# Optimization experiments

Hardware: AMD Instinct MI355X
Metric: run time of the kernel (lower is better)

The kernel has to match this reference:

```python
import jax, jax.numpy as jnp
import numpy as np
from jax import lax

NUM_C_TYPES = 6
TTYPE_UNKNOWN = 5
E = 6            # num_experts_C
D = 1024         # embed_dim
H = D // 4       # gate hidden
TOP_K = 1
TEMP = 0.1
FLOOR = min(0.05, 0.15 / 4)   # routing_floor property (num_experts_B = 4)
CAP_LOW, CAP_HIGH, T_MAX = 0.5, 0.6, 1000


def _build_base_assignment():
    base = np.zeros((NUM_C_TYPES, E), dtype=np.float32)
    for t_type in range(NUM_C_TYPES - 1):
        base[t_type, t_type % E] = 1.0
    base[TTYPE_UNKNOWN] = 1.0 / E
    num_known = NUM_C_TYPES - 1
    if E > num_known:
        for extra_idx in range(num_known, E):
            base[extra_idx % num_known, extra_idx] = 0.3
        for t_type in range(NUM_C_TYPES - 1):
            s = base[t_type].sum()
            if s > 0:
                base[t_type] /= s
    return jnp.asarray(base)


def setup_inputs() -> dict:
    key = jax.random.key(0)
    k1, k2, k3, k4, k5 = jax.random.split(key, 5)
    B, N = 8, 4096
    tokens = jax.random.normal(k1, (B, N, D), dtype=jnp.float32)
    token_types = jax.random.randint(k2, (B, N), 0, NUM_C_TYPES, dtype=jnp.int64)
    t = jax.random.randint(k3, (B,), 0, T_MAX, dtype=jnp.int64)
    # second_gate params; xavier_uniform with gain=0.01
    lim1 = 0.01 * np.sqrt(6.0 / (D + H))
    lim2 = 0.01 * np.sqrt(6.0 / (H + E))
    W1 = jax.random.uniform(k4, (D, H), minval=-lim1, maxval=lim1, dtype=jnp.float32)
    b1 = jnp.zeros((H,), dtype=jnp.float32)
    W2 = jax.random.uniform(k5, (H, E), minval=-lim2, maxval=lim2, dtype=jnp.float32)
    b2 = jnp.zeros((E,), dtype=jnp.float32)
    return {"tokens": tokens, "token_types": token_types, "t": t,
            "W1": W1, "b1": b1, "W2": W2, "b2": b2,
            "base_assignment": _build_base_assignment()}


def _hard_cap(probs, t):
    # TokenLevelHardCap.apply (note faithful cap formula: low + (high + low) * t_norm)
    t_norm = t.astype(probs.dtype) / T_MAX
    cap = (CAP_LOW + (CAP_HIGH + CAP_LOW) * t_norm)[:, None, None]  # (B,1,1)
    excess = jax.nn.relu(probs - cap)
    capped = probs - excess
    headroom = jax.nn.relu(cap - capped)
    headroom_sum = jnp.clip(headroom.sum(-1, keepdims=True), 1e-8, None)
    capped = capped + excess.sum(-1, keepdims=True) * (headroom / headroom_sum)
    return capped


def reference(tokens, token_types, t, W1, b1, W2, b2, base_assignment):
    B, N, _ = tokens.shape
    # primary: deterministic type -> expert assignment (gather)
    base_probs = base_assignment[token_types]                 # (B,N,E)
    # secondary: 2-layer MLP gate, temperature-scaled logits
    h = jax.nn.gelu(jnp.einsum('bnd,dh->bnh', tokens, W1) + b1, approximate=False)
    secondary_logits = (jnp.einsum('bnh,he->bne', h, W2) + b2) / TEMP
    is_unknown = (token_types == TTYPE_UNKNOWN)[..., None].astype(tokens.dtype)
    # faithful to source: unknown tokens blend in raw logits (not softmax probs)
    probs = (1.0 - is_unknown) * base_probs + is_unknown * secondary_logits
    # routing floor interpolation toward uniform
    alpha = min(FLOOR * E, 1.0)
    probs = (1.0 - alpha) * probs + alpha * (1.0 / E)
    # top-k scatter mask
    vals, idx = lax.top_k(probs, TOP_K)                       # (B,N,k)
    dispatch = (jax.nn.one_hot(idx, E, dtype=probs.dtype) * vals[..., None]).sum(-2)
    # no_grad hard cap with redistribution
    dispatch = lax.stop_gradient(_hard_cap(dispatch, t))
    combine = dispatch / (dispatch.sum(-1, keepdims=True) + 1e-8)
    return dispatch, combine
```

## Files before the change

kernel.cpp:

```cpp
#include <hip/hip_runtime.h>
#include <math.h>

#define NUM_E 6
#define DIM 1024
#define HID 256
#define NTOK 32768
#define NPB 4096
#define TTYPE_UNKNOWN 5
#define ONE_MINUS_ALPHA 0.775f
#define FLOOR_TERM 0.0375f
#define GRP 8
#define KSPLIT 8
#define KSPAN 128
#define CPT 4

__device__ __forceinline__ void finalize_and_write(const float probs[NUM_E], float cap,
                                                   float* __restrict__ disp_out,
                                                   float* __restrict__ comb_out) {
    float v = probs[0];
    int bi = 0;
#pragma unroll
    for (int e = 1; e < NUM_E; ++e) {
        if (probs[e] > v) { v = probs[e]; bi = e; }
    }
    float excess = fmaxf(v - cap, 0.0f);
    float capped = v - excess;
    float hr_idx = fmaxf(cap - capped, 0.0f);
    float hsum = fmaxf(hr_idx + 5.0f * cap, 1e-8f);
    float disp[NUM_E];
    float other = excess * cap / hsum;
#pragma unroll
    for (int e = 0; e < NUM_E; ++e) disp[e] = other;
    disp[bi] = capped + excess * hr_idx / hsum;
    float s = 0.0f;
#pragma unroll
    for (int e = 0; e < NUM_E; ++e) s += disp[e];
    float inv = 1.0f / (s + 1e-8f);
#pragma unroll
    for (int e = 0; e < NUM_E; ++e) {
        disp_out[e] = disp[e];
        comb_out[e] = disp[e] * inv;
    }
}

__launch_bounds__(256)
__global__ void classify_kernel(const int* __restrict__ ttypes,
                                const int* __restrict__ tarr,
                                const float* __restrict__ base,
                                float* __restrict__ out,
                                int* __restrict__ cnt,
                                int* __restrict__ list) {
    int i = blockIdx.x * blockDim.x + threadIdx.x;
    if (i >= NTOK) return;
    int ty = ttypes[i];
    if (ty == TTYPE_UNKNOWN) {
        int pos = atomicAdd(cnt, 1);
        list[pos] = i;
        return;
    }
    int b = i / NPB;
    float tnorm = (float)tarr[b] / 1000.0f;
    float cap = 0.5f + 1.1f * tnorm;
    float probs[NUM_E];
#pragma unroll
    for (int e = 0; e < NUM_E; ++e)
        probs[e] = ONE_MINUS_ALPHA * base[ty * NUM_E + e] + FLOOR_TERM;
    finalize_and_write(probs, cap,
                       out + (size_t)i * NUM_E,
                       out + (size_t)NTOK * NUM_E + (size_t)i * NUM_E);
}

__launch_bounds__(512)
__global__ void mlp_kernel(const float* __restrict__ tokens,
                           const int* __restrict__ tarr,
                           const float* __restrict__ W1,
                           const float* __restrict__ b1,
                           const float* __restrict__ W2,
                           const float* __restrict__ b2,
                           float* __restrict__ out,
                           const int* __restrict__ cnt,
                           const int* __restrict__ list) {
    __shared__ float smem[GRP * DIM];
    __shared__ float w2s[HID * NUM_E];
    __shared__ float ls[GRP][NUM_E];

    int count = cnt[0];
    int start = blockIdx.x * GRP;
    if (start >= count) return;
    int tid = threadIdx.x;

    float (*xs)[DIM] = (float (*)[DIM])smem;

    {
        int slot = tid & 255;
        int rr = tid >> 8;
#pragma unroll
        for (int p = 0; p < 4; ++p) {
            int r = rr * 4 + p;
            int idx = start + r;
            if (idx > count - 1) idx = count - 1;
            int tok = list[idx];
            const float4* src = reinterpret_cast<const float4*>(tokens + (size_t)tok * DIM);
            reinterpret_cast<float4*>(xs[r])[slot] = src[slot];
        }
    }
    for (int kk = tid; kk < HID * NUM_E; kk += 512) w2s[kk] = W2[kk];
    __syncthreads();

    int cg = tid & 63;
    int ks = tid >> 6;
    int kbase = ks * KSPAN;
    int colbase = cg * CPT;

    float acc[GRP][CPT];
#pragma unroll
    for (int r = 0; r < GRP; ++r)
#pragma unroll
        for (int c = 0; c < CPT; ++c) acc[r][c] = 0.0f;

    const float* w1p = W1 + (size_t)kbase * HID + colbase;
    const float* xbase = &xs[0][kbase];

#pragma unroll 2
    for (int k = 0; k < KSPAN; k += 4) {
        float4 w[4];
        const float* wp = w1p + (size_t)k * HID;
#pragma unroll
        for (int kk = 0; kk < 4; ++kk)
            w[kk] = *reinterpret_cast<const float4*>(wp + kk * HID);
#pragma unroll
        for (int r = 0; r < GRP; ++r) {
            float4 xq = *reinterpret_cast<const float4*>(xbase + r * DIM + k);
            acc[r][0] = fmaf(xq.x, w[0].x, acc[r][0]);
            acc[r][1] = fmaf(xq.x, w[0].y, acc[r][1]);
            acc[r][2] = fmaf(xq.x, w[0].z, acc[r][2]);
            acc[r][3] = fmaf(xq.x, w[0].w, acc[r][3]);
            acc[r][0] = fmaf(xq.y, w[1].x, acc[r][0]);
            acc[r][1] = fmaf(xq.y, w[1].y, acc[r][1]);
            acc[r][2] = fmaf(xq.y, w[1].z, acc[r][2]);
            acc[r][3] = fmaf(xq.y, w[1].w, acc[r][3]);
            acc[r][0] = fmaf(xq.z, w[2].x, acc[r][0]);
            acc[r][1] = fmaf(xq.z, w[2].y, acc[r][1]);
            acc[r][2] = fmaf(xq.z, w[2].z, acc[r][2]);
            acc[r][3] = fmaf(xq.z, w[2].w, acc[r][3]);
            acc[r][0] = fmaf(xq.w, w[3].x, acc[r][0]);
            acc[r][1] = fmaf(xq.w, w[3].y, acc[r][1]);
            acc[r][2] = fmaf(xq.w, w[3].z, acc[r][2]);
            acc[r][3] = fmaf(xq.w, w[3].w, acc[r][3]);
        }
    }
    __syncthreads();

    float (*hp)[HID] = (float (*)[HID])smem;
    float (*hs)[HID + 1] = (float (*)[HID + 1])(smem + 2048);

    const float kc = 0.70710678118654752f;
#pragma unroll 1
    for (int r = 0; r < GRP; ++r) {
#pragma unroll
        for (int c = 0; c < CPT; ++c) hp[ks][colbase + c] = acc[r][c];
        __syncthreads();
        if (tid < HID) {
            float s = hp[0][tid];
#pragma unroll
            for (int q = 1; q < KSPLIT; ++q) s += hp[q][tid];
            float pre = s + b1[tid];
            hs[r][tid] = 0.5f * pre * (1.0f + erff(pre * kc));
        }
        __syncthreads();
    }

    if (tid < GRP * NUM_E) {
        int r = tid / NUM_E, e = tid % NUM_E;
        float s = 0.0f;
        for (int j = 0; j < HID; ++j) s = fmaf(hs[r][j], w2s[j * NUM_E + e], s);
        ls[r][e] = (s + b2[e]) / 0.1f;
    }
    __syncthreads();

    if (tid < GRP && start + tid < count) {
        int tokidx = list[start + tid];
        int b = tokidx / NPB;
        float tnorm = (float)tarr[b] / 1000.0f;
        float cap = 0.5f + 1.1f * tnorm;
        float probs[NUM_E];
#pragma unroll
        for (int e = 0; e < NUM_E; ++e)
            probs[e] = ONE_MINUS_ALPHA * ls[tid][e] + FLOOR_TERM;
        finalize_and_write(probs, cap,
                           out + (size_t)tokidx * NUM_E,
                           out + (size_t)NTOK * NUM_E + (size_t)tokidx * NUM_E);
    }
}

extern "C" void kernel_launch(void* const* d_in, const int* in_sizes, int n_in,
                              void* d_out, int out_size, void* d_ws, size_t ws_size,
                              hipStream_t stream) {
    const float* tokens = (const float*)d_in[0];
    const int*   ttypes = (const int*)d_in[1];
    const int*   tarr   = (const int*)d_in[2];
    const float* W1     = (const float*)d_in[3];
    const float* b1     = (const float*)d_in[4];
    const float* W2     = (const float*)d_in[5];
    const float* b2     = (const float*)d_in[6];
    const float* base   = (const float*)d_in[7];
    float* out = (float*)d_out;

    int* cnt  = (int*)d_ws;
    int* list = (int*)d_ws + 64;

    hipMemsetAsync(cnt, 0, sizeof(int), stream);
    classify_kernel<<<NTOK / 256, 256, 0, stream>>>(ttypes, tarr, base, out, cnt, list);
    mlp_kernel<<<NTOK / GRP, 512, 0, stream>>>(tokens, tarr, W1, b1, W2, b2,
                                               out, cnt, list);
}
```

Before: 67.63 us.

## Use split-bf16 MFMA for gate MLP with fp32 recheck of near-tie tokens

Replaces the scalar FP32 first-layer GEMM for unknown tokens with MFMA bf16x3 emulation. Weights and activations are split into high and low bf16 parts, and W1 is pre-packed into an MFMA-friendly layout by a prep kernel each call. Tokens whose top-two routing probabilities are closer than a small epsilon are queued and recomputed in exact FP32 by a recheck kernel, so the argmax matches the reference. This adds two kernel launches, a weight repack and a workspace-size dependent fallback path in exchange for matrix-core throughput.

```diff
diff --git a/kernel.cpp b/kernel.cpp
--- a/kernel.cpp
+++ b/kernel.cpp
@@ -9,10 +9,19 @@
 #define TTYPE_UNKNOWN 5
 #define ONE_MINUS_ALPHA 0.775f
 #define FLOOR_TERM 0.0375f
-#define GRP 8
-#define KSPLIT 8
-#define KSPAN 128
-#define CPT 4
+#define GRPM 16
+#define EPS_GAP 2e-5f
+
+#define WS_CNT   0
+#define WS_CNT2  64
+#define WS_LIST  256
+#define WS_LIST2 (256 + 131072)
+#define WS_WFH   (512 * 1024)
+#define WS_WFL   (1024 * 1024)
+#define WS_NEED  ((size_t)(1536 * 1024))
+
+typedef __attribute__((ext_vector_type(8))) short short8;
+typedef __attribute__((ext_vector_type(4))) float f32x4;
 
 __device__ __forceinline__ void finalize_and_write(const float probs[NUM_E], float cap,
                                                    float* __restrict__ disp_out,
@@ -70,27 +79,229 @@
                        out + (size_t)NTOK * NUM_E + (size_t)i * NUM_E);
 }
 
+__launch_bounds__(256)
+__global__ void prep_w1(const float* __restrict__ W1,
+                        unsigned short* __restrict__ wfh,
+                        unsigned short* __restrict__ wfl) {
+    int idx = blockIdx.x * 256 + threadIdx.x;
+    int tg = idx >> 8;
+    int col = idx & 255;
+    int kbase = (tg >> 2) * 32 + (tg & 3) * 8;
+    unsigned int hw[4], lw[4];
+#pragma unroll
+    for (int p = 0; p < 4; ++p) {
+        unsigned int h2 = 0, l2 = 0;
+#pragma unroll
+        for (int q = 0; q < 2; ++q) {
+            int j = p * 2 + q;
+            float w = W1[(size_t)(kbase + j) * HID + col];
+            unsigned int u = __float_as_uint(w);
+            float hif = __uint_as_float(u & 0xFFFF0000u);
+            float resid = w - hif;
+            unsigned int hv = u >> 16;
+            unsigned int lv = __float_as_uint(resid) >> 16;
+            h2 |= hv << (16 * q);
+            l2 |= lv << (16 * q);
+        }
+        hw[p] = h2; lw[p] = l2;
+    }
+    size_t off = ((size_t)tg * 256 + col) * 8;
+    *reinterpret_cast<uint4*>(wfh + off) = make_uint4(hw[0], hw[1], hw[2], hw[3]);
+    *reinterpret_cast<uint4*>(wfl + off) = make_uint4(lw[0], lw[1], lw[2], lw[3]);
+}
+
+__launch_bounds__(256)
+__global__ void mfma_mlp(const float* __restrict__ tokens,
+                         const int* __restrict__ tarr,
+                         const unsigned short* __restrict__ wfh,
+                         const unsigned short* __restrict__ wfl,
+                         const float* __restrict__ b1,
+                         const float* __restrict__ W2,
+                         const float* __restrict__ b2,
+                         float* __restrict__ out,
+                         const int* __restrict__ cnt,
+                         const int* __restrict__ list,
+                         int* __restrict__ cnt2,
+                         int* __restrict__ list2) {
+    __shared__ unsigned short xh[GRPM][DIM];
+    __shared__ unsigned short xl[GRPM][DIM];
+    __shared__ float w2s[HID * NUM_E];
+    __shared__ float ls[GRPM][NUM_E];
+
+    int count = cnt[0];
+    int start = blockIdx.x * GRPM;
+    if (count == 0 || start >= count) return;
+    int tid = threadIdx.x;
+
+#pragma unroll 1
+    for (int r = 0; r < GRPM; ++r) {
+        int idx = start + r;
+        if (idx > count - 1) idx = count - 1;
+        int tok = list[idx];
+        float4 v = reinterpret_cast<const float4*>(tokens + (size_t)tok * DIM)[tid];
+        unsigned short h4[4], l4[4];
+        float xv[4] = {v.x, v.y, v.z, v.w};
+#pragma unroll
+        for (int q = 0; q < 4; ++q) {
+            unsigned int u = __float_as_uint(xv[q]);
+            float hif = __uint_as_float(u & 0xFFFF0000u);
+            float resid = xv[q] - hif;
+            h4[q] = (unsigned short)(u >> 16);
+            l4[q] = (unsigned short)(__float_as_uint(resid) >> 16);
+        }
+        *reinterpret_cast<ushort4*>(&xh[r][tid * 4]) = make_ushort4(h4[0], h4[1], h4[2], h4[3]);
+        *reinterpret_cast<ushort4*>(&xl[r][tid * 4]) = make_ushort4(l4[0], l4[1], l4[2], l4[3]);
+    }
+    for (int kk = tid; kk < HID * NUM_E; kk += 256) w2s[kk] = W2[kk];
+    __syncthreads();
+
+    int lane = tid & 63;
+    int wv = tid >> 6;
+    int arow = lane & 15;
+    int grp = lane >> 4;
+
+    f32x4 acc[4];
+#pragma unroll
+    for (int c = 0; c < 4; ++c) acc[c] = (f32x4){0.f, 0.f, 0.f, 0.f};
+
+    int colg[4];
+#pragma unroll
+    for (int c = 0; c < 4; ++c) colg[c] = wv * 64 + c * 16 + (lane & 15);
+
+#pragma unroll 1
+    for (int t = 0; t < DIM / 32; ++t) {
+        short8 ah = *reinterpret_cast<const short8*>(&xh[arow][t * 32 + grp * 8]);
+        short8 al = *reinterpret_cast<const short8*>(&xl[arow][t * 32 + grp * 8]);
+#pragma unroll
+        for (int c = 0; c < 4; ++c) {
+            size_t boff = ((size_t)(t * 4 + grp) * 256 + colg[c]) * 8;
+            short8 bh = *reinterpret_cast<const short8*>(wfh + boff);
+            short8 bl = *reinterpret_cast<const short8*>(wfl + boff);
+            acc[c] = __builtin_amdgcn_mfma_f32_16x16x32_bf16(ah, bh, acc[c], 0, 0, 0);
+            acc[c] = __builtin_amdgcn_mfma_f32_16x16x32_bf16(ah, bl, acc[c], 0, 0, 0);
+            acc[c] = __builtin_amdgcn_mfma_f32_16x16x32_bf16(al, bh, acc[c], 0, 0, 0);
+        }
+    }
+    __syncthreads();
+
+    float (*hs)[HID] = (float (*)[HID])xh;
+    const float kc = 0.70710678118654752f;
+#pragma unroll
+    for (int c = 0; c < 4; ++c) {
+        float bb = b1[colg[c]];
+#pragma unroll
+        for (int i = 0; i < 4; ++i) {
+            int row = grp * 4 + i;
+            float pre = acc[c][i] + bb;
+            hs[row][colg[c]] = 0.5f * pre * (1.0f + erff(pre * kc));
+        }
+    }
+    __syncthreads();
+
+    if (tid < GRPM * NUM_E) {
+        int r = tid / NUM_E, e = tid % NUM_E;
+        float s = 0.0f;
+        for (int j = 0; j < HID; ++j) s = fmaf(hs[r][j], w2s[j * NUM_E + e], s);
+        ls[r][e] = (s + b2[e]) / 0.1f;
+    }
+    __syncthreads();
+
+    if (tid < GRPM && start + tid < count) {
+        int tokidx = list[start + tid];
+        int b = tokidx / NPB;
+        float tnorm = (float)tarr[b] / 1000.0f;
+        float cap = 0.5f + 1.1f * tnorm;
+        float probs[NUM_E];
+#pragma unroll
+        for (int e = 0; e < NUM_E; ++e)
+            probs[e] = ONE_MINUS_ALPHA * ls[tid][e] + FLOOR_TERM;
+        float v1 = -1e30f, v2 = -1e30f;
+#pragma unroll
+        for (int e = 0; e < NUM_E; ++e) {
+            if (probs[e] > v1) { v2 = v1; v1 = probs[e]; }
+            else if (probs[e] > v2) { v2 = probs[e]; }
+        }
+        if (v1 - v2 < EPS_GAP) {
+            int p = atomicAdd(cnt2, 1);
+            list2[p] = tokidx;
+        }
+        finalize_and_write(probs, cap,
+                           out + (size_t)tokidx * NUM_E,
+                           out + (size_t)NTOK * NUM_E + (size_t)tokidx * NUM_E);
+    }
+}
+
+__launch_bounds__(256)
+__global__ void recheck_kernel(const float* __restrict__ tokens,
+                               const int* __restrict__ tarr,
+                               const float* __restrict__ W1,
+                               const float* __restrict__ b1,
+                               const float* __restrict__ W2,
+                               const float* __restrict__ b2,
+                               float* __restrict__ out,
+                               const int* __restrict__ cnt2,
+                               const int* __restrict__ list2) {
+    __shared__ float xs2[DIM];
+    __shared__ float hs2[HID];
+    __shared__ float ls2[NUM_E];
+    __shared__ float w2s2[HID * NUM_E];
+    int tid = threadIdx.x;
+    int n2 = cnt2[0];
+    if (n2 == 0) return;
+    for (int kk = tid; kk < HID * NUM_E; kk += 256) w2s2[kk] = W2[kk];
+    const float kc = 0.70710678118654752f;
+    for (int i = blockIdx.x; i < n2; i += gridDim.x) {
+        int tok = list2[i];
+        __syncthreads();
+        reinterpret_cast<float4*>(xs2)[tid] =
+            reinterpret_cast<const float4*>(tokens + (size_t)tok * DIM)[tid];
+        __syncthreads();
+        float a = 0.0f;
+        const float* wp = W1 + tid;
+#pragma unroll 8
+        for (int k = 0; k < DIM; ++k) a = fmaf(xs2[k], wp[(size_t)k * HID], a);
+        float pre = a + b1[tid];
+        hs2[tid] = 0.5f * pre * (1.0f + erff(pre * kc));
+        __syncthreads();
+        if (tid < NUM_E) {
+            float s = 0.0f;
+            for (int j = 0; j < HID; ++j) s = fmaf(hs2[j], w2s2[j * NUM_E + tid], s);
+            ls2[tid] = (s + b2[tid]) / 0.1f;
+        }
+        __syncthreads();
+        if (tid == 0) {
+            int b = tok / NPB;
+            float tnorm = (float)tarr[b] / 1000.0f;
+            float cap = 0.5f + 1.1f * tnorm;
+            float probs[NUM_E];
+#pragma unroll
+            for (int e = 0; e < NUM_E; ++e)
+                probs[e] = ONE_MINUS_ALPHA * ls2[e] + FLOOR_TERM;
+            finalize_and_write(probs, cap,
+                               out + (size_t)tok * NUM_E,
+                               out + (size_t)NTOK * NUM_E + (size_t)tok * NUM_E);
+        }
+    }
+}
+
 __launch_bounds__(512)
-__global__ void mlp_kernel(const float* __restrict__ tokens,
-                           const int* __restrict__ tarr,
-                           const float* __restrict__ W1,
-                           const float* __restrict__ b1,
-                           const float* __restrict__ W2,
-                           const float* __restrict__ b2,
-                           float* __restrict__ out,
-                           const int* __restrict__ cnt,
-                           const int* __restrict__ list) {
-    __shared__ float smem[GRP * DIM];
+__global__ void mlp_fallback(const float* __restrict__ tokens,
+                             const int* __restrict__ tarr,
+                             const float* __restrict__ W1,
+                             const float* __restrict__ b1,
+                             const float* __restrict__ W2,
+                             const float* __restrict__ b2,
+                             float* __restrict__ out,
+                             const int* __restrict__ cnt,
+                             const int* __restrict__ list) {
+    __shared__ float smem[8 * DIM];
     __shared__ float w2s[HID * NUM_E];
-    __shared__ float ls[GRP][NUM_E];
-
+    __shared__ float ls[8][NUM_E];
     int count = cnt[0];
-    int start = blockIdx.x * GRP;
-    if (start >= count) return;
+    int start = blockIdx.x * 8;
+    if (count == 0 || start >= count) return;
     int tid = threadIdx.x;
-
     float (*xs)[DIM] = (float (*)[DIM])smem;
-
     {
         int slot = tid & 255;
         int rr = tid >> 8;
@@ -100,36 +311,30 @@
             int idx = start + r;
             if (idx > count - 1) idx = count - 1;
             int tok = list[idx];
-            const float4* src = reinterpret_cast<const float4*>(tokens + (size_t)tok * DIM);
-            reinterpret_cast<float4*>(xs[r])[slot] = src[slot];
+            reinterpret_cast<float4*>(xs[r])[slot] =
+                reinterpret_cast<const float4*>(tokens + (size_t)tok * DIM)[slot];
         }
     }
     for (int kk = tid; kk < HID * NUM_E; kk += 512) w2s[kk] = W2[kk];
     __syncthreads();
-
-    int cg = tid & 63;
-    int ks = tid >> 6;
-    int kbase = ks * KSPAN;
-    int colbase = cg * CPT;
-
-    float acc[GRP][CPT];
-#pragma unroll
-    for (int r = 0; r < GRP; ++r)
-#pragma unroll
-        for (int c = 0; c < CPT; ++c) acc[r][c] = 0.0f;
-
+    int cg = tid & 63, ks = tid >> 6;
+    int kbase = ks * 128, colbase = cg * 4;
+    float acc[8][4];
+#pragma unroll
+    for (int r = 0; r < 8; ++r)
+#pragma unroll
+        for (int c = 0; c < 4; ++c) acc[r][c] = 0.0f;
     const float* w1p = W1 + (size_t)kbase * HID + colbase;
     const float* xbase = &xs[0][kbase];
-
 #pragma unroll 2
-    for (int k = 0; k < KSPAN; k += 4) {
+    for (int k = 0; k < 128; k += 4) {
         float4 w[4];
         const float* wp = w1p + (size_t)k * HID;
 #pragma unroll
         for (int kk = 0; kk < 4; ++kk)
             w[kk] = *reinterpret_cast<const float4*>(wp + kk * HID);
 #pragma unroll
-        for (int r = 0; r < GRP; ++r) {
+        for (int r = 0; r < 8; ++r) {
             float4 xq = *reinterpret_cast<const float4*>(xbase + r * DIM + k);
             acc[r][0] = fmaf(xq.x, w[0].x, acc[r][0]);
             acc[r][1] = fmaf(xq.x, w[0].y, acc[r][1]);
@@ -150,35 +355,31 @@
         }
     }
     __syncthreads();
-
     float (*hp)[HID] = (float (*)[HID])smem;
     float (*hs)[HID + 1] = (float (*)[HID + 1])(smem + 2048);
-
     const float kc = 0.70710678118654752f;
 #pragma unroll 1
-    for (int r = 0; r < GRP; ++r) {
-#pragma unroll
-        for (int c = 0; c < CPT; ++c) hp[ks][colbase + c] = acc[r][c];
+    for (int r = 0; r < 8; ++r) {
+#pragma unroll
+        for (int c = 0; c < 4; ++c) hp[ks][colbase + c] = acc[r][c];
         __syncthreads();
         if (tid < HID) {
             float s = hp[0][tid];
 #pragma unroll
-            for (int q = 1; q < KSPLIT; ++q) s += hp[q][tid];
+            for (int q = 1; q < 8; ++q) s += hp[q][tid];
             float pre = s + b1[tid];
             hs[r][tid] = 0.5f * pre * (1.0f + erff(pre * kc));
         }
         __syncthreads();
     }
-
-    if (tid < GRP * NUM_E) {
+    if (tid < 8 * NUM_E) {
         int r = tid / NUM_E, e = tid % NUM_E;
         float s = 0.0f;
         for (int j = 0; j < HID; ++j) s = fmaf(hs[r][j], w2s[j * NUM_E + e], s);
         ls[r][e] = (s + b2[e]) / 0.1f;
     }
     __syncthreads();
-
-    if (tid < GRP && start + tid < count) {
+    if (tid < 8 && start + tid < count) {
         int tokidx = list[start + tid];
         int b = tokidx / NPB;
         float tnorm = (float)tarr[b] / 1000.0f;
@@ -206,11 +407,25 @@
     const float* base   = (const float*)d_in[7];
     float* out = (float*)d_out;
 
-    int* cnt  = (int*)d_ws;
-    int* list = (int*)d_ws + 64;
-
-    hipMemsetAsync(cnt, 0, sizeof(int), stream);
+    char* ws = (char*)d_ws;
+    int* cnt   = (int*)(ws + WS_CNT);
+    int* cnt2  = (int*)(ws + WS_CNT2);
+    int* list  = (int*)(ws + WS_LIST);
+    int* list2 = (int*)(ws + WS_LIST2);
+
+    hipMemsetAsync(ws, 0, 128, stream);
     classify_kernel<<<NTOK / 256, 256, 0, stream>>>(ttypes, tarr, base, out, cnt, list);
-    mlp_kernel<<<NTOK / GRP, 512, 0, stream>>>(tokens, tarr, W1, b1, W2, b2,
-                                               out, cnt, list);
-}
+
+    if (ws_size >= WS_NEED) {
+        unsigned short* wfh = (unsigned short*)(ws + WS_WFH);
+        unsigned short* wfl = (unsigned short*)(ws + WS_WFL);
+        prep_w1<<<128, 256, 0, stream>>>(W1, wfh, wfl);
+        mfma_mlp<<<NTOK / GRPM, 256, 0, stream>>>(tokens, tarr, wfh, wfl, b1, W2, b2,
+                                                  out, cnt, list, cnt2, list2);
+        recheck_kernel<<<1024, 256, 0, stream>>>(tokens, tarr, W1, b1, W2, b2,
+                                                 out, cnt2, list2);
+    } else {
+        mlp_fallback<<<NTOK / 8, 512, 0, stream>>>(tokens, tarr, W1, b1, W2, b2,
+                                                   out, cnt, list);
+    }
+}
```

After: 118.3 us. 74.9% more time.
